# Optimization experiments

Measured on AMD Instinct MI355X. Metric: run time of the kernel, lower is better.

The kernel has to match this reference:

```python
import jax, jax.numpy as jnp
import numpy as np

B, S, E = 4, 2048, 1024
H, D = 16, 64  # n_heads, head_dim; scale hardcoded as 1/sqrt(64) in source


def setup_inputs() -> dict:
    key = jax.random.key(0)
    ks = jax.random.split(key, 6)
    mk = lambda k, shp, scale=1.0: (jax.random.normal(k, shp, dtype=jnp.float32) * scale)
    return {
        "queries": mk(ks[0], (B, S, E)),
        "keys": mk(ks[1], (B, S, E)),
        "values": mk(ks[2], (B, S, E)),
        "Wq": mk(ks[3], (E, H * D), E ** -0.5),
        "Wk": mk(ks[4], (E, H * D), E ** -0.5),
        "Wv": mk(ks[5], (E, H * D), E ** -0.5),
    }


def reference(queries, keys, values, Wq, Wk, Wv):
    # linear projections
    q = jnp.einsum("bse,ef->bsf", queries, Wq).reshape(B, S, H, D)
    k = jnp.einsum("bse,ef->bsf", keys, Wk).reshape(B, S, H, D)
    v = jnp.einsum("bse,ef->bsf", values, Wv).reshape(B, S, H, D)
    # scaled dot-product attention per head (scale hardcoded to 1/sqrt(64) in source)
    scores = jnp.einsum("bqhd,bkhd->bhqk", q, k) * (1.0 / np.sqrt(64.0)).astype(np.float32)
    weights = jax.nn.softmax(scores, axis=-1)
    ctx = jnp.einsum("bhqk,bkhd->bqhd", weights, v)
    # merge heads back: [B, S, H*D]
    return ctx.reshape(B, S, H * D)
```

## Files before the change

### kernel.cpp

```cpp
#include <hip/hip_runtime.h>
#include <math.h>

#define SEQ 2048
#define EMB 1024
#define NH 16
#define HD 64
#define BH 64
#define L2E 1.44269504088896340736f

typedef __attribute__((ext_vector_type(8))) short bf16x8;
typedef __attribute__((ext_vector_type(4))) float f32x4;
typedef __attribute__((ext_vector_type(16))) float f32x16;
typedef __attribute__((ext_vector_type(4))) unsigned short u16x4;

__device__ __forceinline__ unsigned short f2bf(float f) {
  union { float fv; unsigned u; } v; v.fv = f;
  return (unsigned short)((v.u + 0x7FFFu + ((v.u >> 16) & 1u)) >> 16);
}

__device__ __forceinline__ unsigned cvt_pk_bf16(float lo, float hi) {
  unsigned r;
  asm("v_cvt_pk_bf16_f32 %0, %1, %2" : "=v"(r) : "v"(lo), "v"(hi));
  return r;
}

__device__ __forceinline__ void gl_lds16(const void* g, void* l) {
  __builtin_amdgcn_global_load_lds(
      (const __attribute__((address_space(1))) unsigned*)g,
      (__attribute__((address_space(3))) unsigned*)l, 16, 0, 0);
}

__global__ __launch_bounds__(256) void k_wt3(const float* __restrict__ Wq,
                                             const float* __restrict__ Wk,
                                             const float* __restrict__ Wv,
                                             unsigned short* __restrict__ tq,
                                             unsigned short* __restrict__ tk,
                                             unsigned short* __restrict__ tv) {
  int z = blockIdx.z;
  const float* W = (z == 0) ? Wq : (z == 1) ? Wk : Wv;
  unsigned short* Wt = (z == 0) ? tq : (z == 1) ? tk : tv;
  const float scale = (z == 0) ? 0.125f * L2E : 1.0f;

  __shared__ float tile[32][33];
  int j0 = blockIdx.x * 32, i0 = blockIdx.y * 32;
  int tx = threadIdx.x & 31, ty = threadIdx.x >> 5;
#pragma unroll
  for (int r = 0; r < 32; r += 8)
    tile[ty + r][tx] = W[(i0 + ty + r) * EMB + j0 + tx];
  __syncthreads();
#pragma unroll
  for (int r = 0; r < 32; r += 8)
    Wt[(j0 + ty + r) * EMB + i0 + tx] = f2bf(tile[tx][ty + r] * scale);
}

__global__ __launch_bounds__(256) void k_proj(
    const float* __restrict__ xq, const float* __restrict__ xk,
    const float* __restrict__ xv,
    const unsigned short* __restrict__ w0, const unsigned short* __restrict__ w1,
    const unsigned short* __restrict__ w2,
    unsigned short* __restrict__ o0, unsigned short* __restrict__ o1,
    unsigned short* __restrict__ o2) {
  int z = blockIdx.z;
  const float* X = (z == 0) ? xq : (z == 1) ? xk : xv;
  const unsigned short* Wt = (z == 0) ? w0 : (z == 1) ? w1 : w2;
  unsigned short* O = (z == 0) ? o0 : (z == 1) ? o1 : o2;

  __shared__ __align__(16) unsigned short As[2][128 * 64];
  __shared__ __align__(16) unsigned short Bs[2][128 * 64];

  int tid = threadIdx.x;
  int lane = tid & 63, w = tid >> 6;
  int ln15 = lane & 15, lg = lane >> 4;
  int wr = w >> 1, wc = w & 1;
  int row0 = blockIdx.x * 128, col0 = blockIdx.y * 128;

  const char* Xb = (const char*)X;
  const char* Wb = (const char*)Wt;

  f32x4 acc[4][4];
#pragma unroll
  for (int i = 0; i < 4; ++i)
#pragma unroll
    for (int j = 0; j < 4; ++j) acc[i][j] = (f32x4){0.f, 0.f, 0.f, 0.f};

  int oc[4], dswz[4];
  size_t srcA[4];
#pragma unroll
  for (int c = 0; c < 4; ++c) {
    oc[c] = w * 4096 + c * 1024 + lane * 16;
    dswz[c] = oc[c] ^ (((oc[c] >> 7) & 7) << 4);
    srcA[c] = (size_t)(row0 + (oc[c] >> 7)) * (EMB * 4) + (size_t)(oc[c] & 127) * 2;
  }
  int soB[4];
#pragma unroll
  for (int c = 0; c < 4; ++c) soB[c] = oc[c] ^ (((oc[c] >> 7) & 7) << 4);

  f32x4 ar[4][2];
  auto ldA = [&](int kt) {
#pragma unroll
    for (int c = 0; c < 4; ++c) {
      const char* p = Xb + srcA[c] + kt * 256;
      ar[c][0] = *(const f32x4*)p;
      ar[c][1] = *(const f32x4*)(p + 16);
    }
  };
  auto wrA = [&](int buf) {
#pragma unroll
    for (int c = 0; c < 4; ++c) {
      union { unsigned u[4]; bf16x8 v; } pk;
      pk.u[0] = cvt_pk_bf16(ar[c][0][0], ar[c][0][1]);
      pk.u[1] = cvt_pk_bf16(ar[c][0][2], ar[c][0][3]);
      pk.u[2] = cvt_pk_bf16(ar[c][1][0], ar[c][1][1]);
      pk.u[3] = cvt_pk_bf16(ar[c][1][2], ar[c][1][3]);
      *(bf16x8*)((char*)As[buf] + dswz[c]) = pk.v;
    }
  };
  auto stageB = [&](int buf, int kt) {
#pragma unroll
    for (int c = 0; c < 4; ++c)
      gl_lds16(Wb + (size_t)(col0 + (soB[c] >> 7)) * (EMB * 2) + kt * 128 + (soB[c] & 127),
               (char*)Bs[buf] + w * 4096 + c * 1024);
  };

  ldA(0);
  stageB(0, 0);
  wrA(0);
  __syncthreads();

  for (int kt = 0; kt < 16; ++kt) {
    int cur = kt & 1;
    if (kt < 15) {
      ldA(kt + 1);
      stageB(cur ^ 1, kt + 1);
    }

#pragma unroll
    for (int ks = 0; ks < 2; ++ks) {
      bf16x8 a[4], bb[4];
#pragma unroll
      for (int i = 0; i < 4; ++i) {
        int row = wr * 64 + i * 16 + ln15;
        int ba = (row * 128 + ks * 64 + lg * 16) ^ ((row & 7) << 4);
        a[i] = *(const bf16x8*)((const char*)As[cur] + ba);
      }
#pragma unroll
      for (int j = 0; j < 4; ++j) {
        int row = wc * 64 + j * 16 + ln15;
        int ba = (row * 128 + ks * 64 + lg * 16) ^ ((row & 7) << 4);
        bb[j] = *(const bf16x8*)((const char*)Bs[cur] + ba);
      }
      __builtin_amdgcn_s_setprio(1);
#pragma unroll
      for (int i = 0; i < 4; ++i)
#pragma unroll
        for (int j = 0; j < 4; ++j)
          acc[i][j] = __builtin_amdgcn_mfma_f32_16x16x32_bf16(a[i], bb[j], acc[i][j], 0, 0, 0);
      __builtin_amdgcn_s_setprio(0);
    }
    if (kt < 15) wrA(cur ^ 1);
    __syncthreads();
  }

  if (z == 2) {
#pragma unroll
    for (int i = 0; i < 4; ++i) {
#pragma unroll
      for (int j = 0; j < 4; ++j) {
        int col = col0 + wc * 64 + j * 16 + ln15;
        int h = col >> 6, d = col & 63;
        int rowb = row0 + wr * 64 + i * 16 + lg * 4;
        int b = rowb >> 11, s = rowb & (SEQ - 1);
        u16x4 hv;
#pragma unroll
        for (int r = 0; r < 4; ++r) hv[r] = f2bf(acc[i][j][r]);
        *(u16x4*)&O[(((size_t)(b * NH + h) * HD) + d) * SEQ + s] = hv;
      }
    }
  } else {
#pragma unroll
    for (int i = 0; i < 4; ++i) {
#pragma unroll
      for (int j = 0; j < 4; ++j) {
#pragma unroll
        for (int r = 0; r < 4; ++r) {
          int row = row0 + wr * 64 + i * 16 + lg * 4 + r;
          int col = col0 + wc * 64 + j * 16 + ln15;
          int b = row >> 11, s = row & (SEQ - 1);
          int h = col >> 6, d = col & 63;
          O[(((size_t)(b * NH + h) * SEQ) + s) * HD + d] = f2bf(acc[i][j][r]);
        }
      }
    }
  }
}

__global__ __launch_bounds__(512) void k_attn(const unsigned short* __restrict__ Q,
                                              const unsigned short* __restrict__ K,
                                              const unsigned short* __restrict__ Vt,
                                              float* __restrict__ out) {
  __shared__ __align__(16) unsigned short Klds[2 * 32 * 64];
  __shared__ __align__(16) unsigned short Vlds[2 * 64 * 64];

  const int id = blockIdx.x;
  const int swz = (id & 7) * 64 + (id >> 3);
  const int bh = swz >> 3, qb = swz & 7;
  const int b = bh >> 4, h = bh & 15;

  const int tid = threadIdx.x;
  const int w = tid >> 6, lane = tid & 63;
  const int q31 = lane & 31;
  const int hi = lane >> 5;
  const int q0 = qb * 256 + w * 32;

  const unsigned short* Qb = Q + (size_t)bh * SEQ * HD;
  const char* Kb = (const char*)(K + (size_t)bh * SEQ * HD);
  const char* Vb = (const char*)(Vt + (size_t)bh * HD * SEQ);

  bf16x8 qf[4];
#pragma unroll
  for (int kk = 0; kk < 4; ++kk)
    qf[kk] = *(const bf16x8*)&Qb[(q0 + q31) * HD + kk * 16 + hi * 8];

  f32x16 ctx[2];
#pragma unroll
  for (int db = 0; db < 2; ++db)
#pragma unroll
    for (int r = 0; r < 16; ++r) ctx[db][r] = 0.f;

  f32x16 zero16;
#pragma unroll
  for (int r = 0; r < 16; ++r) zero16[r] = 0.f;
  union { unsigned u[4]; bf16x8 v; } onesf;
#pragma unroll
  for (int r = 0; r < 4; ++r) onesf.u[r] = 0x3F803F80u;
  f32x16 lsum = zero16;

  const int sw = (q31 & 7) << 4;
  int kaddr[4];
#pragma unroll
  for (int kk = 0; kk < 4; ++kk)
    kaddr[kk] = q31 * 128 + (((kk * 32) | (hi * 16)) ^ sw);
  int vaddr[2][2];
#pragma unroll
  for (int pi = 0; pi < 2; ++pi)
#pragma unroll
    for (int j = 0; j < 2; ++j)
      vaddr[pi][j] = q31 * 128 + (((pi * 64) | (j * 32) | (hi * 16)) ^ sw);

  const int o0 = w * 1024 + lane * 16;
  const int os0 = o0 ^ (((o0 >> 7) & 7) << 4);

  auto stageK = [&](int slot, int kt) {
    if (w < 4)
      gl_lds16(Kb + (size_t)kt * 4096 + os0, (char*)Klds + slot * 4096 + w * 1024);
  };
  auto stageV = [&](int slot, int vt) {
    gl_lds16(Vb + (size_t)(os0 >> 7) * (SEQ * 2) + vt * 128 + (os0 & 127),
             (char*)Vlds + slot * 8192 + w * 1024);
  };

  auto barrierC = [&]() {
    if (w < 4) asm volatile("s_waitcnt vmcnt(1)" ::: "memory");
    __builtin_amdgcn_s_barrier();
    __builtin_amdgcn_sched_barrier(0);
  };

  auto qk = [&](f32x16& sx, const char* kbase) {
    __builtin_amdgcn_s_setprio(1);
    bf16x8 kf0 = *(const bf16x8*)(kbase + kaddr[0]);
    sx = __builtin_amdgcn_mfma_f32_32x32x16_bf16(kf0, qf[0], zero16, 0, 0, 0);
#pragma unroll
    for (int kk = 1; kk < 4; ++kk) {
      bf16x8 kf = *(const bf16x8*)(kbase + kaddr[kk]);
      sx = __builtin_amdgcn_mfma_f32_32x32x16_bf16(kf, qf[kk], sx, 0, 0, 0);
    }
    __builtin_amdgcn_s_setprio(0);
  };

  auto smpv = [&](f32x16& sx, int pinIdx, int vb) {
#pragma unroll
    for (int r = 0; r < 16; ++r) sx[r] = __builtin_amdgcn_exp2f(sx[r]);

    unsigned a0 = cvt_pk_bf16(sx[0], sx[1]);
    unsigned a1 = cvt_pk_bf16(sx[2], sx[3]);
    unsigned a2 = cvt_pk_bf16(sx[4], sx[5]);
    unsigned a3 = cvt_pk_bf16(sx[6], sx[7]);
    unsigned a4 = cvt_pk_bf16(sx[8], sx[9]);
    unsigned a5 = cvt_pk_bf16(sx[10], sx[11]);
    unsigned a6 = cvt_pk_bf16(sx[12], sx[13]);
    unsigned a7 = cvt_pk_bf16(sx[14], sx[15]);
    asm volatile("v_permlane32_swap_b32 %0, %1" : "+v"(a0), "+v"(a2));
    asm volatile("v_permlane32_swap_b32 %0, %1" : "+v"(a1), "+v"(a3));
    asm volatile("v_permlane32_swap_b32 %0, %1" : "+v"(a4), "+v"(a6));
    asm volatile("v_permlane32_swap_b32 %0, %1" : "+v"(a5), "+v"(a7));
    union { unsigned u[4]; bf16x8 v; } pa_lo, pa_hi;
    pa_lo.u[0] = a0; pa_lo.u[1] = a1; pa_lo.u[2] = a2; pa_lo.u[3] = a3;
    pa_hi.u[0] = a4; pa_hi.u[1] = a5; pa_hi.u[2] = a6; pa_hi.u[3] = a7;

    const char* vbp = (const char*)Vlds + vb;
    __builtin_amdgcn_s_setprio(1);
    lsum = __builtin_amdgcn_mfma_f32_32x32x16_bf16(pa_lo.v, onesf.v, lsum, 0, 0, 0);
    lsum = __builtin_amdgcn_mfma_f32_32x32x16_bf16(pa_hi.v, onesf.v, lsum, 0, 0, 0);
#pragma unroll
    for (int db = 0; db < 2; ++db) {
      bf16x8 v0 = *(const bf16x8*)(vbp + db * 4096 + vaddr[pinIdx][0]);
      bf16x8 v1 = *(const bf16x8*)(vbp + db * 4096 + vaddr[pinIdx][1]);
      ctx[db] = __builtin_amdgcn_mfma_f32_32x32x16_bf16(pa_lo.v, v0, ctx[db], 0, 0, 0);
      ctx[db] = __builtin_amdgcn_mfma_f32_32x32x16_bf16(pa_hi.v, v1, ctx[db], 0, 0, 0);
    }
    __builtin_amdgcn_s_setprio(0);
  };

  const char* K0 = (const char*)Klds;
  const char* K1 = (const char*)Klds + 4096;
  f32x16 sA, sB;

  stageK(0, 0);
  stageV(0, 0);
  barrierC();
  qk(sA, K0);
  stageK(1, 1);
  __syncthreads();

  for (int tp = 0; tp < 31; ++tp) {
    const int vb = (tp & 1) << 13;
    qk(sB, K1);
    stageK(0, 2 * tp + 2);
    stageV((tp + 1) & 1, tp + 1);
    smpv(sA, 0, vb);
    barrierC();
    qk(sA, K0);
    stageK(1, 2 * tp + 3);
    smpv(sB, 1, vb);
    __syncthreads();
  }
  qk(sB, K1);
  smpv(sA, 0, 8192);
  smpv(sB, 1, 8192);

#pragma unroll
  for (int db = 0; db < 2; ++db) {
#pragma unroll
    for (int r = 0; r < 16; ++r) {
      int q = q0 + (r & 3) + 8 * (r >> 2) + 4 * hi;
      out[((size_t)b * SEQ + q) * (NH * HD) + h * HD + db * 32 + q31] =
          ctx[db][r] / lsum[r];
    }
  }
}

extern "C" void kernel_launch(void* const* d_in, const int* in_sizes, int n_in,
                              void* d_out, int out_size, void* d_ws, size_t ws_size,
                              hipStream_t stream) {
  (void)in_sizes; (void)n_in; (void)out_size; (void)ws_size;
  const float* queries = (const float*)d_in[0];
  const float* keys    = (const float*)d_in[1];
  const float* values  = (const float*)d_in[2];
  const float* Wq = (const float*)d_in[3];
  const float* Wk = (const float*)d_in[4];
  const float* Wv = (const float*)d_in[5];
  float* out = (float*)d_out;

  char* ws = (char*)d_ws;
  const size_t MB = 1024 * 1024;
  unsigned short* q_ws = (unsigned short*)(ws);
  unsigned short* k_ws = (unsigned short*)(ws + 16 * MB);
  unsigned short* v_ws = (unsigned short*)(ws + 32 * MB);
  unsigned short* wtq  = (unsigned short*)(ws + 48 * MB);
  unsigned short* wtk  = (unsigned short*)(ws + 50 * MB);
  unsigned short* wtv  = (unsigned short*)(ws + 52 * MB);

  k_wt3<<<dim3(32, 32, 3), 256, 0, stream>>>(Wq, Wk, Wv, wtq, wtk, wtv);
  k_proj<<<dim3(64, 8, 3), 256, 0, stream>>>(queries, keys, values,
                                             wtq, wtk, wtv, q_ws, k_ws, v_ws);
  k_attn<<<dim3(512), 512, 0, stream>>>(q_ws, k_ws, v_ws, out);
}
```

Before: 169.5 us.

## Stage fp32 activations directly to LDS and convert to bf16 at fragment load

The projection GEMM now copies the fp32 activation tile straight into shared memory with direct global-to-LDS loads, as the weights already were, instead of loading it into registers, converting to bf16 and writing it out. The K tile drops from 64 to 32 per stage so the fp32 tile fits in the same LDS budget, which doubles the loop trip count and the barrier count. Conversion to bf16 moves to after the LDS read, so each wave converts the fragments it uses and the same A data is converted by more than one wave. The intent is to cut register pressure and the register round-trip on the activation path, at the cost of twice the LDS traffic for A and more synchronisation.

```diff
diff --git a/kernel.cpp b/kernel.cpp
--- a/kernel.cpp
+++ b/kernel.cpp
@@ -65,8 +65,8 @@
   const unsigned short* Wt = (z == 0) ? w0 : (z == 1) ? w1 : w2;
   unsigned short* O = (z == 0) ? o0 : (z == 1) ? o1 : o2;
 
-  __shared__ __align__(16) unsigned short As[2][128 * 64];
-  __shared__ __align__(16) unsigned short Bs[2][128 * 64];
+  __shared__ __align__(16) float As[2][128 * 32];
+  __shared__ __align__(16) unsigned short Bs[2][128 * 32];
 
   int tid = threadIdx.x;
   int lane = tid & 63, w = tid >> 6;
@@ -83,81 +83,65 @@
 #pragma unroll
     for (int j = 0; j < 4; ++j) acc[i][j] = (f32x4){0.f, 0.f, 0.f, 0.f};
 
-  int oc[4], dswz[4];
-  size_t srcA[4];
+  int soA[4];
 #pragma unroll
   for (int c = 0; c < 4; ++c) {
-    oc[c] = w * 4096 + c * 1024 + lane * 16;
-    dswz[c] = oc[c] ^ (((oc[c] >> 7) & 7) << 4);
-    srcA[c] = (size_t)(row0 + (oc[c] >> 7)) * (EMB * 4) + (size_t)(oc[c] & 127) * 2;
-  }
-  int soB[4];
-#pragma unroll
-  for (int c = 0; c < 4; ++c) soB[c] = oc[c] ^ (((oc[c] >> 7) & 7) << 4);
-
-  f32x4 ar[4][2];
-  auto ldA = [&](int kt) {
-#pragma unroll
-    for (int c = 0; c < 4; ++c) {
-      const char* p = Xb + srcA[c] + kt * 256;
-      ar[c][0] = *(const f32x4*)p;
-      ar[c][1] = *(const f32x4*)(p + 16);
-    }
-  };
-  auto wrA = [&](int buf) {
-#pragma unroll
-    for (int c = 0; c < 4; ++c) {
+    int o = c * 4096 + w * 1024 + lane * 16;
+    soA[c] = o ^ (((o >> 7) & 7) << 4);
+  }
+  int soB[2];
+#pragma unroll
+  for (int c = 0; c < 2; ++c) {
+    int o = c * 4096 + w * 1024 + lane * 16;
+    soB[c] = o ^ (((o >> 6) & 3) << 4);
+  }
+
+  auto stage = [&](int buf, int kt) {
+#pragma unroll
+    for (int c = 0; c < 4; ++c)
+      gl_lds16(Xb + (size_t)(row0 + (soA[c] >> 7)) * (EMB * 4) + kt * 128 + (soA[c] & 127),
+               (char*)As[buf] + c * 4096 + w * 1024);
+#pragma unroll
+    for (int c = 0; c < 2; ++c)
+      gl_lds16(Wb + (size_t)(col0 + (soB[c] >> 6)) * (EMB * 2) + kt * 64 + (soB[c] & 63),
+               (char*)Bs[buf] + c * 4096 + w * 1024);
+  };
+
+  stage(0, 0);
+  __syncthreads();
+
+  for (int kt = 0; kt < 32; ++kt) {
+    int cur = kt & 1;
+    if (kt < 31) stage(cur ^ 1, kt + 1);
+
+    bf16x8 a[4], bb[4];
+#pragma unroll
+    for (int i = 0; i < 4; ++i) {
+      int row = wr * 64 + i * 16 + ln15;
+      int sw7 = (row & 7) << 4;
+      const char* base = (const char*)As[cur];
+      f32x4 fl = *(const f32x4*)(base + ((row * 128 + lg * 32) ^ sw7));
+      f32x4 fh = *(const f32x4*)(base + ((row * 128 + lg * 32 + 16) ^ sw7));
       union { unsigned u[4]; bf16x8 v; } pk;
-      pk.u[0] = cvt_pk_bf16(ar[c][0][0], ar[c][0][1]);
-      pk.u[1] = cvt_pk_bf16(ar[c][0][2], ar[c][0][3]);
-      pk.u[2] = cvt_pk_bf16(ar[c][1][0], ar[c][1][1]);
-      pk.u[3] = cvt_pk_bf16(ar[c][1][2], ar[c][1][3]);
-      *(bf16x8*)((char*)As[buf] + dswz[c]) = pk.v;
-    }
-  };
-  auto stageB = [&](int buf, int kt) {
-#pragma unroll
-    for (int c = 0; c < 4; ++c)
-      gl_lds16(Wb + (size_t)(col0 + (soB[c] >> 7)) * (EMB * 2) + kt * 128 + (soB[c] & 127),
-               (char*)Bs[buf] + w * 4096 + c * 1024);
-  };
-
-  ldA(0);
-  stageB(0, 0);
-  wrA(0);
-  __syncthreads();
-
-  for (int kt = 0; kt < 16; ++kt) {
-    int cur = kt & 1;
-    if (kt < 15) {
-      ldA(kt + 1);
-      stageB(cur ^ 1, kt + 1);
-    }
-
-#pragma unroll
-    for (int ks = 0; ks < 2; ++ks) {
-      bf16x8 a[4], bb[4];
-#pragma unroll
-      for (int i = 0; i < 4; ++i) {
-        int row = wr * 64 + i * 16 + ln15;
-        int ba = (row * 128 + ks * 64 + lg * 16) ^ ((row & 7) << 4);
-        a[i] = *(const bf16x8*)((const char*)As[cur] + ba);
-      }
-#pragma unroll
-      for (int j = 0; j < 4; ++j) {
-        int row = wc * 64 + j * 16 + ln15;
-        int ba = (row * 128 + ks * 64 + lg * 16) ^ ((row & 7) << 4);
-        bb[j] = *(const bf16x8*)((const char*)Bs[cur] + ba);
-      }
-      __builtin_amdgcn_s_setprio(1);
-#pragma unroll
-      for (int i = 0; i < 4; ++i)
-#pragma unroll
-        for (int j = 0; j < 4; ++j)
-          acc[i][j] = __builtin_amdgcn_mfma_f32_16x16x32_bf16(a[i], bb[j], acc[i][j], 0, 0, 0);
-      __builtin_amdgcn_s_setprio(0);
-    }
-    if (kt < 15) wrA(cur ^ 1);
+      pk.u[0] = cvt_pk_bf16(fl[0], fl[1]);
+      pk.u[1] = cvt_pk_bf16(fl[2], fl[3]);
+      pk.u[2] = cvt_pk_bf16(fh[0], fh[1]);
+      pk.u[3] = cvt_pk_bf16(fh[2], fh[3]);
+      a[i] = pk.v;
+    }
+#pragma unroll
+    for (int j = 0; j < 4; ++j) {
+      int row = wc * 64 + j * 16 + ln15;
+      int ba = (row * 64 + lg * 16) ^ ((row & 3) << 4);
+      bb[j] = *(const bf16x8*)((const char*)Bs[cur] + ba);
+    }
+    __builtin_amdgcn_s_setprio(1);
+#pragma unroll
+    for (int i = 0; i < 4; ++i)
+#pragma unroll
+      for (int j = 0; j < 4; ++j)
+        acc[i][j] = __builtin_amdgcn_mfma_f32_16x16x32_bf16(a[i], bb[j], acc[i][j], 0, 0, 0);
+    __builtin_amdgcn_s_setprio(0);
     __syncthreads();
   }
 
```

New measurement: 185.4 us. 9.4% more time.

## Deepen A-operand prefetch to two tiles ahead with ping-pong registers

Applied to the files above, without the earlier changes.

The projection GEMM's main loop now keeps two register sets for the fp32 A tiles and unrolls the k loop by two. Global loads for tile k+2 are issued while tile k is being multiplied, so load latency is hidden over a longer window. The cost is roughly double the VGPRs for the A staging registers, which may lower occupancy, plus a fully unrolled loop that grows code size.

```diff
diff --git a/kernel.cpp b/kernel.cpp
--- a/kernel.cpp
+++ b/kernel.cpp
@@ -95,23 +95,42 @@
 #pragma unroll
   for (int c = 0; c < 4; ++c) soB[c] = oc[c] ^ (((oc[c] >> 7) & 7) << 4);
 
-  f32x4 ar[4][2];
-  auto ldA = [&](int kt) {
+  f32x4 arA[4][2], arB[4][2];
+  auto ldA_A = [&](int kt) {
 #pragma unroll
     for (int c = 0; c < 4; ++c) {
       const char* p = Xb + srcA[c] + kt * 256;
-      ar[c][0] = *(const f32x4*)p;
-      ar[c][1] = *(const f32x4*)(p + 16);
-    }
-  };
-  auto wrA = [&](int buf) {
+      arA[c][0] = *(const f32x4*)p;
+      arA[c][1] = *(const f32x4*)(p + 16);
+    }
+  };
+  auto ldA_B = [&](int kt) {
+#pragma unroll
+    for (int c = 0; c < 4; ++c) {
+      const char* p = Xb + srcA[c] + kt * 256;
+      arB[c][0] = *(const f32x4*)p;
+      arB[c][1] = *(const f32x4*)(p + 16);
+    }
+  };
+  auto wrA_A = [&](int buf) {
 #pragma unroll
     for (int c = 0; c < 4; ++c) {
       union { unsigned u[4]; bf16x8 v; } pk;
-      pk.u[0] = cvt_pk_bf16(ar[c][0][0], ar[c][0][1]);
-      pk.u[1] = cvt_pk_bf16(ar[c][0][2], ar[c][0][3]);
-      pk.u[2] = cvt_pk_bf16(ar[c][1][0], ar[c][1][1]);
-      pk.u[3] = cvt_pk_bf16(ar[c][1][2], ar[c][1][3]);
+      pk.u[0] = cvt_pk_bf16(arA[c][0][0], arA[c][0][1]);
+      pk.u[1] = cvt_pk_bf16(arA[c][0][2], arA[c][0][3]);
+      pk.u[2] = cvt_pk_bf16(arA[c][1][0], arA[c][1][1]);
+      pk.u[3] = cvt_pk_bf16(arA[c][1][2], arA[c][1][3]);
+      *(bf16x8*)((char*)As[buf] + dswz[c]) = pk.v;
+    }
+  };
+  auto wrA_B = [&](int buf) {
+#pragma unroll
+    for (int c = 0; c < 4; ++c) {
+      union { unsigned u[4]; bf16x8 v; } pk;
+      pk.u[0] = cvt_pk_bf16(arB[c][0][0], arB[c][0][1]);
+      pk.u[1] = cvt_pk_bf16(arB[c][0][2], arB[c][0][3]);
+      pk.u[2] = cvt_pk_bf16(arB[c][1][0], arB[c][1][1]);
+      pk.u[3] = cvt_pk_bf16(arB[c][1][2], arB[c][1][3]);
       *(bf16x8*)((char*)As[buf] + dswz[c]) = pk.v;
     }
   };
@@ -122,18 +141,7 @@
                (char*)Bs[buf] + w * 4096 + c * 1024);
   };
 
-  ldA(0);
-  stageB(0, 0);
-  wrA(0);
-  __syncthreads();
-
-  for (int kt = 0; kt < 16; ++kt) {
-    int cur = kt & 1;
-    if (kt < 15) {
-      ldA(kt + 1);
-      stageB(cur ^ 1, kt + 1);
-    }
-
+  auto mfmaStep = [&](int cur) {
 #pragma unroll
     for (int ks = 0; ks < 2; ++ks) {
       bf16x8 a[4], bb[4];
@@ -157,7 +165,28 @@
           acc[i][j] = __builtin_amdgcn_mfma_f32_16x16x32_bf16(a[i], bb[j], acc[i][j], 0, 0, 0);
       __builtin_amdgcn_s_setprio(0);
     }
-    if (kt < 15) wrA(cur ^ 1);
+  };
+
+  ldA_A(0);
+  stageB(0, 0);
+  wrA_A(0);
+  ldA_B(1);
+  __syncthreads();
+
+#pragma unroll
+  for (int kp = 0; kp < 8; ++kp) {
+    const int kte = 2 * kp;
+    stageB(1, kte + 1);
+    if (kte < 14) ldA_A(kte + 2);
+    mfmaStep(0);
+    wrA_B(1);
+    __syncthreads();
+
+    const int kto = 2 * kp + 1;
+    if (kto < 15) stageB(0, kto + 1);
+    if (kto < 14) ldA_B(kto + 2);
+    mfmaStep(1);
+    if (kto < 15) wrA_A(0);
     __syncthreads();
   }
 
```

Measured after the change: 159.8 us. 5.8% less time.
